# Kernel optimization log

Measured on AMD Instinct MI355X. Metric: run time of the kernel, lower is better.

Reference implementation:

```python
import jax, jax.numpy as jnp
import numpy as np

B, I, J, N, C, H = 1, 256, 64, 384, 256, 8
CH = C // H  # per-head channels
EPS = 1e-5


def layer_norm(x, scale, bias):
    mu = jnp.mean(x, axis=-1, keepdims=True)
    var = jnp.mean(jnp.square(x - mu), axis=-1, keepdims=True)
    return (x - mu) * jax.lax.rsqrt(var + EPS) * scale + bias


def setup_inputs() -> dict:
    key = jax.random.key(0)
    ks = jax.random.split(key, 12)
    s = 0.02
    return {
        "rigids_embed": jax.random.normal(ks[0], (B, I, N, C), dtype=jnp.float32),
        "rigids_memory": jax.random.normal(ks[1], (J, N, C), dtype=jnp.float32),
        "rigids_mask": jax.random.randint(ks[2], (B, I, N), 0, 2, dtype=jnp.int32),
        "memory_mask": jax.random.randint(ks[3], (J, N), 0, 2, dtype=jnp.int32),
        "ln_q_scale": jnp.ones((C,), jnp.float32),
        "ln_q_bias": jnp.zeros((C,), jnp.float32),
        "ln_kv_scale": jnp.ones((C,), jnp.float32),
        "ln_kv_bias": jnp.zeros((C,), jnp.float32),
        "Wq": jax.random.normal(ks[4], (C, C), dtype=jnp.float32) * s,
        "Wkv": jax.random.normal(ks[5], (C, 2 * C), dtype=jnp.float32) * s,
        "Wgate": jax.random.normal(ks[6], (C, C), dtype=jnp.float32) * s,
        "Wout": jax.random.normal(ks[7], (C, C), dtype=jnp.float32) * s,
        "ln_ffn_scale": jnp.ones((C,), jnp.float32),
        "ln_ffn_bias": jnp.zeros((C,), jnp.float32),
        "W1": jax.random.normal(ks[8], (C, 2 * C), dtype=jnp.float32) * s,
        "b1": jnp.zeros((2 * C,), jnp.float32),
        "W2": jax.random.normal(ks[9], (2 * C, C), dtype=jnp.float32) * s,
        "b2": jnp.zeros((C,), jnp.float32),
    }


def reference(rigids_embed, rigids_memory, rigids_mask, memory_mask,
              ln_q_scale, ln_q_bias, ln_kv_scale, ln_kv_bias,
              Wq, Wkv, Wgate, Wout,
              ln_ffn_scale, ln_ffn_bias, W1, b1, W2, b2):
    rmask = rigids_mask.astype(jnp.float32)   # [B,I,N]
    mmask = memory_mask.astype(jnp.float32)   # [J,N]

    # ---- gated cross-attention ----
    qe = layer_norm(rigids_embed, ln_q_scale, ln_q_bias)      # [B,I,N,C]
    km = layer_norm(rigids_memory, ln_kv_scale, ln_kv_bias)   # [J,N,C]

    # mask: [B,I,1,N] * [1,1,J,N] -> [B,I,J,N]
    mask = rmask[:, :, None, :] * mmask[None, None]

    q = (qe @ Wq).reshape(B, I, N, H, CH)                      # [B,I,N,H,CH]
    kv = (km @ Wkv).reshape(J, N, 2 * H, CH)                   # [J,N,2H,CH]
    k, v = kv[:, :, :H, :], kv[:, :, H:, :]                    # [J,N,H,CH] each

    a = jnp.einsum('binhc,jnhc->bijnh', q, k)                  # [B,I,J,N,H]
    a = a + (mask[..., None] - 1.0) * 1e6
    a = jax.nn.softmax(a, axis=-1)  # NOTE: softmax over heads, as in source

    out = jnp.einsum('bijnh,jnhc->binhc', a, v)                # [B,I,N,H,CH]
    gate = (qe @ Wgate).reshape(out.shape)
    out = out * jax.nn.sigmoid(gate)
    out = out.reshape(B, I, N, C) @ Wout
    out = out * rmask[..., None]

    x = rigids_embed + out

    # ---- Transition FFN (LN -> Linear(C,2C) -> ReLU -> Linear(2C,C)) ----
    h = layer_norm(x, ln_ffn_scale, ln_ffn_bias)
    h = jax.nn.relu(h @ W1 + b1) @ W2 + b2
    x = x + h * rmask[..., None]
    return x
```

## Files before the change

### kernel.cpp

```cpp
#include <hip/hip_runtime.h>
#include <math.h>

using u16 = unsigned short;
using u32 = unsigned int;

typedef __attribute__((ext_vector_type(4))) float f32x4;
typedef __attribute__((ext_vector_type(8))) short s16x8;

__device__ __forceinline__ u16 f2bf(float f) {
  union { float f; u32 u; } c; c.f = f;
  u32 u = c.u;
  u += 0x7fffu + ((u >> 16) & 1u);
  return (u16)(u >> 16);
}
__device__ __forceinline__ float bf2f(u16 s) {
  union { u32 u; float f; } c; c.u = ((u32)s) << 16;
  return c.f;
}
__device__ __forceinline__ void async16(const void* g, void* l) {
  __builtin_amdgcn_global_load_lds(
      (const __attribute__((address_space(1))) void*)g,
      (__attribute__((address_space(3))) void*)l, 16, 0, 0);
}

__global__ __launch_bounds__(256) void ln_kernel(
    const float* __restrict__ x, const float* __restrict__ sc,
    const float* __restrict__ bi, u16* __restrict__ out) {
  const int w = threadIdx.x >> 6, l = threadIdx.x & 63;
  const int row = blockIdx.x * 4 + w;
  const float4 v = ((const float4*)(x + (size_t)row * 256))[l];
  float s  = v.x + v.y + v.z + v.w;
  float s2 = v.x * v.x + v.y * v.y + v.z * v.z + v.w * v.w;
#pragma unroll
  for (int m = 1; m < 64; m <<= 1) {
    s  += __shfl_xor(s,  m, 64);
    s2 += __shfl_xor(s2, m, 64);
  }
  const float mean = s * (1.0f / 256.0f);
  const float var  = s2 * (1.0f / 256.0f) - mean * mean;
  const float rs   = rsqrtf(var + 1e-5f);
  const float4 s4 = ((const float4*)sc)[l];
  const float4 b4 = ((const float4*)bi)[l];
  u16 o0 = f2bf((v.x - mean) * rs * s4.x + b4.x);
  u16 o1 = f2bf((v.y - mean) * rs * s4.y + b4.y);
  u16 o2 = f2bf((v.z - mean) * rs * s4.z + b4.z);
  u16 o3 = f2bf((v.w - mean) * rs * s4.w + b4.w);
  uint2 p; p.x = (u32)o0 | ((u32)o1 << 16); p.y = (u32)o2 | ((u32)o3 << 16);
  *(uint2*)(out + (size_t)row * 256 + l * 4) = p;
}

__global__ __launch_bounds__(256) void convw_kernel(
    const float* s0, const float* s1, const float* s2, const float* s3,
    const float* s4, const float* s5,
    u16* d0, u16* d1, u16* d2, u16* d3, u16* d4, u16* d5) {
  const float* s; u16* d; int K, N, sh;
  switch (blockIdx.y) {
    case 0: s = s0; d = d0; K = 256; N = 256; sh = 8; break;
    case 1: s = s1; d = d1; K = 256; N = 256; sh = 8; break;
    case 2: s = s2; d = d2; K = 256; N = 512; sh = 9; break;
    case 3: s = s3; d = d3; K = 256; N = 256; sh = 8; break;
    case 4: s = s4; d = d4; K = 256; N = 512; sh = 9; break;
    default: s = s5; d = d5; K = 512; N = 256; sh = 8; break;
  }
  const int idx = blockIdx.x * 256 + threadIdx.x;
  if (idx >= K * N) return;
  const int k = idx >> sh, n = idx & (N - 1);
  d[(size_t)n * K + k] = f2bf(s[idx]);
}

__global__ __launch_bounds__(256) void vtrans_kernel(const u16* __restrict__ KV,
                                                     u16* __restrict__ VT) {
  const int n = blockIdx.x, h = blockIdx.y;
  const int t = threadIdx.x;
  const int j = t >> 2, cg = t & 3;
  union { uint4 v; u16 u[8]; } d;
  d.v = *(const uint4*)(KV + ((size_t)(j * 384 + n)) * 512 + 256 + h * 32 + cg * 8);
  u16* dst = VT + (((size_t)n * 8 + h) * 32 + cg * 8) * 64 + j;
#pragma unroll
  for (int c = 0; c < 8; c++) dst[c * 64] = d.u[c];
}

__global__ __launch_bounds__(256) void gemm_kernel(
    const u16* __restrict__ A, const u16* __restrict__ BT,
    const int K, const int N,
    u16* __restrict__ outb, float* __restrict__ outf,
    const float* __restrict__ bias, const float* __restrict__ res,
    const int* __restrict__ rmask, const int epi) {
  __shared__ u16 Als[128 * 32];
  __shared__ u16 Bls[128 * 32];
  const int t = threadIdx.x, w = t >> 6, l = t & 63;
  const int mb = blockIdx.y * 128, nb = blockIdx.x * 128;
  const int lm = l & 15, lk = l >> 4;

  const int cg = (l & 3) ^ ((l >> 3) & 3);
  const int rA = w * 32 + (l >> 2);
  const u16* gA = A  + (size_t)(mb + rA) * K + cg * 8;
  const u16* gB = BT + (size_t)(nb + rA) * K + cg * 8;
  u16* lA0 = &Als[(w * 32) * 32];
  u16* lA1 = &Als[(w * 32 + 16) * 32];
  u16* lB0 = &Bls[(w * 32) * 32];
  u16* lB1 = &Bls[(w * 32 + 16) * 32];
  const size_t rk16 = (size_t)16 * K;

  const int pc = (lk ^ ((l >> 1) & 3)) * 8;
  const int m0 = (w >> 1) * 64, n0 = (w & 1) * 64;

  f32x4 acc[4][4] = {};

  for (int kk = 0; kk < K; kk += 32) {
    if (kk) __syncthreads();
    async16(gA + kk, lA0);
    async16(gA + rk16 + kk, lA1);
    async16(gB + kk, lB0);
    async16(gB + rk16 + kk, lB1);
    __syncthreads();
    s16x8 a[4], b[4];
#pragma unroll
    for (int i = 0; i < 4; i++) a[i] = *(const s16x8*)&Als[(m0 + i * 16 + lm) * 32 + pc];
#pragma unroll
    for (int j = 0; j < 4; j++) b[j] = *(const s16x8*)&Bls[(n0 + j * 16 + lm) * 32 + pc];
#pragma unroll
    for (int i = 0; i < 4; i++)
#pragma unroll
      for (int j = 0; j < 4; j++)
        acc[i][j] = __builtin_amdgcn_mfma_f32_16x16x32_bf16(a[i], b[j], acc[i][j], 0, 0, 0);
  }

  const int r0 = mb + m0 + lk * 4;
  const int c0 = nb + n0 + lm;
  if (epi == 0) {
#pragma unroll
    for (int i = 0; i < 4; i++)
#pragma unroll
      for (int j = 0; j < 4; j++)
#pragma unroll
        for (int r = 0; r < 4; r++)
          outb[(size_t)(r0 + i * 16 + r) * N + (c0 + j * 16)] = f2bf(acc[i][j][r]);
  } else if (epi == 1) {
#pragma unroll
    for (int i = 0; i < 4; i++)
#pragma unroll
      for (int j = 0; j < 4; j++)
#pragma unroll
        for (int r = 0; r < 4; r++) {
          const int col = c0 + j * 16;
          const float v = fmaxf(acc[i][j][r] + bias[col], 0.0f);
          outb[(size_t)(r0 + i * 16 + r) * N + col] = f2bf(v);
        }
  } else if (epi == 2) {
#pragma unroll
    for (int i = 0; i < 4; i++)
#pragma unroll
      for (int r = 0; r < 4; r++) {
        const int row = r0 + i * 16 + r;
        const float rm = (float)rmask[row];
#pragma unroll
        for (int j = 0; j < 4; j++) {
          const size_t idx = (size_t)row * N + (c0 + j * 16);
          outf[idx] = res[idx] + acc[i][j][r] * rm;
        }
      }
  } else {
#pragma unroll
    for (int i = 0; i < 4; i++)
#pragma unroll
      for (int r = 0; r < 4; r++) {
        const int row = r0 + i * 16 + r;
        const float rm = (float)rmask[row];
#pragma unroll
        for (int j = 0; j < 4; j++) {
          const int col = c0 + j * 16;
          const size_t idx = (size_t)row * N + col;
          outf[idx] = outf[idx] + (acc[i][j][r] + bias[col]) * rm;
        }
      }
  }
}

__global__ __launch_bounds__(256) void attn_kernel(
    const u16* __restrict__ QG, const u16* __restrict__ KV,
    const u16* __restrict__ VT, u16* __restrict__ O) {
  __shared__ u16 P[8][16][72];
  const int n = blockIdx.x, ig = blockIdx.y;
  const int t = threadIdx.x, w = t >> 6, l = t & 63;
  const int lm = l & 15, lk = l >> 4;

  const u16* qb = QG + ((size_t)(ig * 16 + lm) * 384 + n) * 512 + lk * 8;
  const u16* kb = KV + ((size_t)(w * 16 + lm) * 384 + n) * 512 + lk * 8;
  const f32x4 zz = {0.f, 0.f, 0.f, 0.f};
  f32x4 acc[8];
#pragma unroll
  for (int h = 0; h < 8; h++) {
    s16x8 af = *(const s16x8*)(qb + h * 32);
    s16x8 bf = *(const s16x8*)(kb + h * 32);
    acc[h] = __builtin_amdgcn_mfma_f32_16x16x32_bf16(af, bf, zz, 0, 0, 0);
  }
#pragma unroll
  for (int r = 0; r < 4; r++) {
    float mx = acc[0][r];
#pragma unroll
    for (int h = 1; h < 8; h++) mx = fmaxf(mx, acc[h][r]);
    float e[8], s = 0.f;
#pragma unroll
    for (int h = 0; h < 8; h++) { e[h] = __expf(acc[h][r] - mx); s += e[h]; }
    const float inv = 1.0f / s;
#pragma unroll
    for (int h = 0; h < 8; h++) P[h][lk * 4 + r][w * 16 + lm] = f2bf(e[h] * inv);
  }
  __syncthreads();

  const u16* vb = VT + ((size_t)n * 8) * 2048;
#pragma unroll
  for (int hh = 0; hh < 2; hh++) {
    const int h = w * 2 + hh;
#pragma unroll
    for (int nt = 0; nt < 2; nt++) {
      f32x4 o = zz;
#pragma unroll
      for (int ks = 0; ks < 2; ks++) {
        s16x8 af = *(const s16x8*)&P[h][lm][ks * 32 + lk * 8];
        s16x8 bf = *(const s16x8*)(vb + (size_t)h * 2048 + (nt * 16 + lm) * 64 + ks * 32 + lk * 8);
        o = __builtin_amdgcn_mfma_f32_16x16x32_bf16(af, bf, o, 0, 0, 0);
      }
#pragma unroll
      for (int r = 0; r < 4; r++) {
        const int i = ig * 16 + lk * 4 + r;
        const int col = h * 32 + nt * 16 + lm;
        const size_t orow = (size_t)i * 384 + n;
        const float g = bf2f(QG[orow * 512 + 256 + col]);
        const float val = o[r] / (1.0f + __expf(-g));
        O[orow * 256 + col] = f2bf(val);
      }
    }
  }
}

extern "C" void kernel_launch(void* const* d_in, const int* in_sizes, int n_in,
                              void* d_out, int out_size, void* d_ws, size_t ws_size,
                              hipStream_t stream) {
  (void)in_sizes; (void)n_in; (void)out_size; (void)ws_size;
  const float* embed  = (const float*)d_in[0];
  const float* memory = (const float*)d_in[1];
  const int*   rmask  = (const int*)d_in[2];
  const float* lnqs = (const float*)d_in[4];
  const float* lnqb = (const float*)d_in[5];
  const float* lnks = (const float*)d_in[6];
  const float* lnkb = (const float*)d_in[7];
  const float* Wq   = (const float*)d_in[8];
  const float* Wkv  = (const float*)d_in[9];
  const float* Wg   = (const float*)d_in[10];
  const float* Wo   = (const float*)d_in[11];
  const float* lnfs = (const float*)d_in[12];
  const float* lnfb = (const float*)d_in[13];
  const float* W1   = (const float*)d_in[14];
  const float* b1   = (const float*)d_in[15];
  const float* W2   = (const float*)d_in[16];
  const float* b2   = (const float*)d_in[17];
  float* out = (float*)d_out;
  char* ws = (char*)d_ws;

  u16* qe   = (u16*)(ws + 0);
  u16* km   = (u16*)(ws + 50331648);
  u16* VT   = km;
  u16* QG   = (u16*)(ws + 62914560);
  u16* h1   = QG;
  u16* KV   = (u16*)(ws + 163577856);
  u16* O    = (u16*)(ws + 188743680);
  u16* WQGT = (u16*)(ws + 239075328);
  u16* WKVT = WQGT + 131072;
  u16* WOUTT= WKVT + 131072;
  u16* W1T  = WOUTT + 65536;
  u16* W2T  = W1T + 131072;
  u16* lnx  = qe;

  convw_kernel<<<dim3(512, 6), 256, 0, stream>>>(Wq, Wg, Wkv, Wo, W1, W2,
      WQGT, WQGT + 65536, WKVT, WOUTT, W1T, W2T);
  ln_kernel<<<24576, 256, 0, stream>>>(embed, lnqs, lnqb, qe);
  ln_kernel<<<6144, 256, 0, stream>>>(memory, lnks, lnkb, km);
  gemm_kernel<<<dim3(4, 768), 256, 0, stream>>>(qe, WQGT, 256, 512, QG, nullptr, nullptr, nullptr, nullptr, 0);
  gemm_kernel<<<dim3(4, 192), 256, 0, stream>>>(km, WKVT, 256, 512, KV, nullptr, nullptr, nullptr, nullptr, 0);
  vtrans_kernel<<<dim3(384, 8), 256, 0, stream>>>(KV, VT);
  attn_kernel<<<dim3(384, 16), 256, 0, stream>>>(QG, KV, VT, O);
  gemm_kernel<<<dim3(2, 768), 256, 0, stream>>>(O, WOUTT, 256, 256, nullptr, out, nullptr, embed, rmask, 2);
  ln_kernel<<<24576, 256, 0, stream>>>(out, lnfs, lnfb, lnx);
  gemm_kernel<<<dim3(4, 768), 256, 0, stream>>>(lnx, W1T, 256, 512, h1, nullptr, b1, nullptr, nullptr, 1);
  gemm_kernel<<<dim3(2, 768), 256, 0, stream>>>(h1, W2T, 512, 256, nullptr, out, b2, nullptr, rmask, 3);
}
```

Baseline: 654.6 us.

## Double-buffer GEMM LDS tiles and remap workgroups across XCDs

The GEMM kernel gets double-buffered LDS for its A and B tiles, so the async global-to-LDS loads for the next K slice are issued before the MFMAs on the current slice, with one barrier per iteration. It also remaps workgroup IDs so consecutive tiles are spread round-robin across the eight XCDs, aiming for better L2 locality. The cost is twice the LDS footprint, which may lower occupancy. The remap assumes gridDim.x is a power of two.

New measurement: 629.0 us. 1.04x faster.

```diff
diff --git a/kernel.cpp b/kernel.cpp
--- a/kernel.cpp
+++ b/kernel.cpp
@@ -86,44 +86,60 @@
     u16* __restrict__ outb, float* __restrict__ outf,
     const float* __restrict__ bias, const float* __restrict__ res,
     const int* __restrict__ rmask, const int epi) {
-  __shared__ u16 Als[128 * 32];
-  __shared__ u16 Bls[128 * 32];
+  __shared__ u16 Als[2][128 * 32];
+  __shared__ u16 Bls[2][128 * 32];
   const int t = threadIdx.x, w = t >> 6, l = t & 63;
-  const int mb = blockIdx.y * 128, nb = blockIdx.x * 128;
   const int lm = l & 15, lk = l >> 4;
+
+  const int nwg = gridDim.x * gridDim.y;
+  const int hw = blockIdx.y * gridDim.x + blockIdx.x;
+  int wid = hw;
+  if (!(nwg & 7)) wid = (hw & 7) * (nwg >> 3) + (hw >> 3);
+  const int gxsh = __builtin_ctz(gridDim.x);
+  const int nb = (wid & (gridDim.x - 1)) * 128;
+  const int mb = (wid >> gxsh) * 128;
 
   const int cg = (l & 3) ^ ((l >> 3) & 3);
   const int rA = w * 32 + (l >> 2);
   const u16* gA = A  + (size_t)(mb + rA) * K + cg * 8;
   const u16* gB = BT + (size_t)(nb + rA) * K + cg * 8;
-  u16* lA0 = &Als[(w * 32) * 32];
-  u16* lA1 = &Als[(w * 32 + 16) * 32];
-  u16* lB0 = &Bls[(w * 32) * 32];
-  u16* lB1 = &Bls[(w * 32 + 16) * 32];
   const size_t rk16 = (size_t)16 * K;
+  const int lofs = (w * 32) * 32;
 
   const int pc = (lk ^ ((l >> 1) & 3)) * 8;
   const int m0 = (w >> 1) * 64, n0 = (w & 1) * 64;
 
   f32x4 acc[4][4] = {};
 
-  for (int kk = 0; kk < K; kk += 32) {
-    if (kk) __syncthreads();
-    async16(gA + kk, lA0);
-    async16(gA + rk16 + kk, lA1);
-    async16(gB + kk, lB0);
-    async16(gB + rk16 + kk, lB1);
-    __syncthreads();
+  async16(gA,        &Als[0][lofs]);
+  async16(gA + rk16, &Als[0][lofs + 16 * 32]);
+  async16(gB,        &Bls[0][lofs]);
+  async16(gB + rk16, &Bls[0][lofs + 16 * 32]);
+  __syncthreads();
+
+  const int nk = K >> 5;
+  int buf = 0;
+  for (int tt = 0; tt < nk; ++tt) {
+    if (tt + 1 < nk) {
+      const int kk = (tt + 1) << 5;
+      const int nbuf = buf ^ 1;
+      async16(gA + kk,        &Als[nbuf][lofs]);
+      async16(gA + rk16 + kk, &Als[nbuf][lofs + 16 * 32]);
+      async16(gB + kk,        &Bls[nbuf][lofs]);
+      async16(gB + rk16 + kk, &Bls[nbuf][lofs + 16 * 32]);
+    }
     s16x8 a[4], b[4];
 #pragma unroll
-    for (int i = 0; i < 4; i++) a[i] = *(const s16x8*)&Als[(m0 + i * 16 + lm) * 32 + pc];
-#pragma unroll
-    for (int j = 0; j < 4; j++) b[j] = *(const s16x8*)&Bls[(n0 + j * 16 + lm) * 32 + pc];
+    for (int i = 0; i < 4; i++) a[i] = *(const s16x8*)&Als[buf][(m0 + i * 16 + lm) * 32 + pc];
+#pragma unroll
+    for (int j = 0; j < 4; j++) b[j] = *(const s16x8*)&Bls[buf][(n0 + j * 16 + lm) * 32 + pc];
 #pragma unroll
     for (int i = 0; i < 4; i++)
 #pragma unroll
       for (int j = 0; j < 4; j++)
         acc[i][j] = __builtin_amdgcn_mfma_f32_16x16x32_bf16(a[i], b[j], acc[i][j], 0, 0, 0);
+    __syncthreads();
+    buf ^= 1;
   }
 
   const int r0 = mb + m0 + lk * 4;
```

## Restructure GEMM to 128x256 tiles with register A, fuse FFN layernorm into out-proj

Applied to the files above, without the earlier changes.

Rewrites the GEMM kernel to use 512-thread blocks computing 128x256 output tiles. A fragments are loaded directly from global memory into registers, and only the weight tile is staged in LDS with an XOR swizzle. Workgroup IDs are remapped across XCDs. The output-projection GEMM (256 columns, one tile per row block) now computes the FFN layernorm in its epilogue, which removes a separate LN kernel and its re-read of the fp32 activations. In exchange, the kernel holds 64 accumulator registers per thread and loses LDS reuse of A across waves.

Measured after the change: 723.2 us. 10.5% more time.

```diff
diff --git a/kernel.cpp b/kernel.cpp
--- a/kernel.cpp
+++ b/kernel.cpp
@@ -80,100 +80,130 @@
   for (int c = 0; c < 8; c++) dst[c * 64] = d.u[c];
 }
 
-__global__ __launch_bounds__(256) void gemm_kernel(
+__global__ __launch_bounds__(512, 4) void gemm_kernel(
     const u16* __restrict__ A, const u16* __restrict__ BT,
     const int K, const int N,
     u16* __restrict__ outb, float* __restrict__ outf,
     const float* __restrict__ bias, const float* __restrict__ res,
-    const int* __restrict__ rmask, const int epi) {
-  __shared__ u16 Als[128 * 32];
-  __shared__ u16 Bls[128 * 32];
+    const int* __restrict__ rmask, const int epi,
+    const float* __restrict__ lns, const float* __restrict__ lnb,
+    u16* __restrict__ lnout) {
+  __shared__ u16 Wls[256 * 64];
   const int t = threadIdx.x, w = t >> 6, l = t & 63;
-  const int mb = blockIdx.y * 128, nb = blockIdx.x * 128;
   const int lm = l & 15, lk = l >> 4;
 
-  const int cg = (l & 3) ^ ((l >> 3) & 3);
-  const int rA = w * 32 + (l >> 2);
-  const u16* gA = A  + (size_t)(mb + rA) * K + cg * 8;
-  const u16* gB = BT + (size_t)(nb + rA) * K + cg * 8;
-  u16* lA0 = &Als[(w * 32) * 32];
-  u16* lA1 = &Als[(w * 32 + 16) * 32];
-  u16* lB0 = &Bls[(w * 32) * 32];
-  u16* lB1 = &Bls[(w * 32 + 16) * 32];
-  const size_t rk16 = (size_t)16 * K;
-
-  const int pc = (lk ^ ((l >> 1) & 3)) * 8;
-  const int m0 = (w >> 1) * 64, n0 = (w & 1) * 64;
-
-  f32x4 acc[4][4] = {};
-
-  for (int kk = 0; kk < K; kk += 32) {
-    if (kk) __syncthreads();
-    async16(gA + kk, lA0);
-    async16(gA + rk16 + kk, lA1);
-    async16(gB + kk, lB0);
-    async16(gB + rk16 + kk, lB1);
+  const int nwg = gridDim.x * gridDim.y;
+  const int hw = blockIdx.y * gridDim.x + blockIdx.x;
+  const int wid = (hw & 7) * (nwg >> 3) + (hw >> 3);
+  const int gxm = gridDim.x - 1;
+  const int gxsh = (gridDim.x == 2) ? 1 : 0;
+  const int nb = (wid & gxm) * 256;
+  const int mb = (wid >> gxsh) * 128;
+  const int KH = K >> 6;
+
+  const u16* arow = A + (size_t)(mb + w * 16 + lm) * K + lk * 8;
+
+  const u16* wl = &Wls[lm * 64];
+  const int swz = lm & 7;
+
+  f32x4 acc[16] = {};
+
+  for (int kh = 0; kh < KH; ++kh) {
+    s16x8 av[2];
+#pragma unroll
+    for (int kcl = 0; kcl < 2; ++kcl)
+      av[kcl] = *(const s16x8*)(arow + kh * 64 + kcl * 32);
+
+    if (kh) __syncthreads();
+#pragma unroll
+    for (int i = 0; i < 4; ++i) {
+      const int s = w * 64 + i * 512 + l;
+      const int n = s >> 3, cl = s & 7;
+      const int g = cl ^ (n & 7);
+      async16(BT + (size_t)(nb + n) * K + kh * 64 + g * 8,
+              &Wls[(w * 64 + i * 512) * 8]);
+    }
     __syncthreads();
-    s16x8 a[4], b[4];
-#pragma unroll
-    for (int i = 0; i < 4; i++) a[i] = *(const s16x8*)&Als[(m0 + i * 16 + lm) * 32 + pc];
-#pragma unroll
-    for (int j = 0; j < 4; j++) b[j] = *(const s16x8*)&Bls[(n0 + j * 16 + lm) * 32 + pc];
-#pragma unroll
-    for (int i = 0; i < 4; i++)
-#pragma unroll
-      for (int j = 0; j < 4; j++)
-        acc[i][j] = __builtin_amdgcn_mfma_f32_16x16x32_bf16(a[i], b[j], acc[i][j], 0, 0, 0);
-  }
-
-  const int r0 = mb + m0 + lk * 4;
-  const int c0 = nb + n0 + lm;
+
+#pragma unroll
+    for (int kcl = 0; kcl < 2; ++kcl) {
+      const int so = (((kcl << 2) | lk) ^ swz) << 3;
+#pragma unroll
+      for (int nt = 0; nt < 16; ++nt) {
+        const s16x8 bv = *(const s16x8*)(wl + nt * 1024 + so);
+        acc[nt] = __builtin_amdgcn_mfma_f32_16x16x32_bf16(av[kcl], bv, acc[nt], 0, 0, 0);
+      }
+    }
+  }
+
+  const int rowb = mb + w * 16 + lk * 4;
+  const int colb = nb + lm;
   if (epi == 0) {
 #pragma unroll
-    for (int i = 0; i < 4; i++)
-#pragma unroll
-      for (int j = 0; j < 4; j++)
-#pragma unroll
-        for (int r = 0; r < 4; r++)
-          outb[(size_t)(r0 + i * 16 + r) * N + (c0 + j * 16)] = f2bf(acc[i][j][r]);
+    for (int nt = 0; nt < 16; ++nt) {
+      const int col = colb + nt * 16;
+#pragma unroll
+      for (int r = 0; r < 4; ++r)
+        outb[(size_t)(rowb + r) * N + col] = f2bf(acc[nt][r]);
+    }
   } else if (epi == 1) {
 #pragma unroll
-    for (int i = 0; i < 4; i++)
-#pragma unroll
-      for (int j = 0; j < 4; j++)
-#pragma unroll
-        for (int r = 0; r < 4; r++) {
-          const int col = c0 + j * 16;
-          const float v = fmaxf(acc[i][j][r] + bias[col], 0.0f);
-          outb[(size_t)(r0 + i * 16 + r) * N + col] = f2bf(v);
-        }
+    for (int nt = 0; nt < 16; ++nt) {
+      const int col = colb + nt * 16;
+      const float bb = bias[col];
+#pragma unroll
+      for (int r = 0; r < 4; ++r)
+        outb[(size_t)(rowb + r) * N + col] = f2bf(fmaxf(acc[nt][r] + bb, 0.0f));
+    }
   } else if (epi == 2) {
-#pragma unroll
-    for (int i = 0; i < 4; i++)
-#pragma unroll
-      for (int r = 0; r < 4; r++) {
-        const int row = r0 + i * 16 + r;
-        const float rm = (float)rmask[row];
-#pragma unroll
-        for (int j = 0; j < 4; j++) {
-          const size_t idx = (size_t)row * N + (c0 + j * 16);
-          outf[idx] = res[idx] + acc[i][j][r] * rm;
-        }
-      }
+    float rm4[4];
+#pragma unroll
+    for (int r = 0; r < 4; ++r) rm4[r] = (float)rmask[rowb + r];
+#pragma unroll
+    for (int nt = 0; nt < 16; ++nt) {
+      const int col = colb + nt * 16;
+#pragma unroll
+      for (int r = 0; r < 4; ++r) {
+        const size_t idx = (size_t)(rowb + r) * N + col;
+        const float x = res[idx] + acc[nt][r] * rm4[r];
+        acc[nt][r] = x;
+        outf[idx] = x;
+      }
+    }
+#pragma unroll
+    for (int r = 0; r < 4; ++r) {
+      float s = 0.f, s2 = 0.f;
+#pragma unroll
+      for (int nt = 0; nt < 16; ++nt) { const float v = acc[nt][r]; s += v; s2 += v * v; }
+#pragma unroll
+      for (int m = 1; m < 16; m <<= 1) {
+        s  += __shfl_xor(s,  m, 64);
+        s2 += __shfl_xor(s2, m, 64);
+      }
+      const float mu = s * (1.0f / 256.0f);
+      const float var = s2 * (1.0f / 256.0f) - mu * mu;
+      const float rs = rsqrtf(var + 1e-5f);
+#pragma unroll
+      for (int nt = 0; nt < 16; ++nt) {
+        const int col = colb + nt * 16;
+        const float v = (acc[nt][r] - mu) * rs * lns[col] + lnb[col];
+        lnout[(size_t)(rowb + r) * N + col] = f2bf(v);
+      }
+    }
   } else {
-#pragma unroll
-    for (int i = 0; i < 4; i++)
-#pragma unroll
-      for (int r = 0; r < 4; r++) {
-        const int row = r0 + i * 16 + r;
-        const float rm = (float)rmask[row];
-#pragma unroll
-        for (int j = 0; j < 4; j++) {
-          const int col = c0 + j * 16;
-          const size_t idx = (size_t)row * N + col;
-          outf[idx] = outf[idx] + (acc[i][j][r] + bias[col]) * rm;
-        }
-      }
+    float rm4[4];
+#pragma unroll
+    for (int r = 0; r < 4; ++r) rm4[r] = (float)rmask[rowb + r];
+#pragma unroll
+    for (int nt = 0; nt < 16; ++nt) {
+      const int col = colb + nt * 16;
+      const float bb = bias[col];
+#pragma unroll
+      for (int r = 0; r < 4; ++r) {
+        const size_t idx = (size_t)(rowb + r) * N + col;
+        outf[idx] = outf[idx] + (acc[nt][r] + bb) * rm4[r];
+      }
+    }
   }
 }
 
@@ -277,12 +307,16 @@
       WQGT, WQGT + 65536, WKVT, WOUTT, W1T, W2T);
   ln_kernel<<<24576, 256, 0, stream>>>(embed, lnqs, lnqb, qe);
   ln_kernel<<<6144, 256, 0, stream>>>(memory, lnks, lnkb, km);
-  gemm_kernel<<<dim3(4, 768), 256, 0, stream>>>(qe, WQGT, 256, 512, QG, nullptr, nullptr, nullptr, nullptr, 0);
-  gemm_kernel<<<dim3(4, 192), 256, 0, stream>>>(km, WKVT, 256, 512, KV, nullptr, nullptr, nullptr, nullptr, 0);
+  gemm_kernel<<<dim3(2, 768), 512, 0, stream>>>(qe, WQGT, 256, 512, QG, nullptr,
+      nullptr, nullptr, nullptr, 0, nullptr, nullptr, nullptr);
+  gemm_kernel<<<dim3(2, 192), 512, 0, stream>>>(km, WKVT, 256, 512, KV, nullptr,
+      nullptr, nullptr, nullptr, 0, nullptr, nullptr, nullptr);
   vtrans_kernel<<<dim3(384, 8), 256, 0, stream>>>(KV, VT);
   attn_kernel<<<dim3(384, 16), 256, 0, stream>>>(QG, KV, VT, O);
-  gemm_kernel<<<dim3(2, 768), 256, 0, stream>>>(O, WOUTT, 256, 256, nullptr, out, nullptr, embed, rmask, 2);
-  ln_kernel<<<24576, 256, 0, stream>>>(out, lnfs, lnfb, lnx);
-  gemm_kernel<<<dim3(4, 768), 256, 0, stream>>>(lnx, W1T, 256, 512, h1, nullptr, b1, nullptr, nullptr, 1);
-  gemm_kernel<<<dim3(2, 768), 256, 0, stream>>>(h1, W2T, 512, 256, nullptr, out, b2, nullptr, rmask, 3);
-}
+  gemm_kernel<<<dim3(1, 768), 512, 0, stream>>>(O, WOUTT, 256, 256, nullptr, out,
+      nullptr, embed, rmask, 2, lnfs, lnfb, lnx);
+  gemm_kernel<<<dim3(2, 768), 512, 0, stream>>>(lnx, W1T, 256, 512, h1, nullptr,
+      b1, nullptr, nullptr, 1, nullptr, nullptr, nullptr);
+  gemm_kernel<<<dim3(1, 768), 512, 0, stream>>>(h1, W2T, 512, 256, nullptr, out,
+      b2, nullptr, rmask, 3, nullptr, nullptr, nullptr);
+}
```
